# Optimization experiments

Measured on AMD Instinct MI355X. Metric: run time of the kernel, lower is better.

The kernel has to match this reference:

```python
import jax, jax.numpy as jnp
import numpy as np

N = 1536
NUM_SPECIES = 8
HIDDEN = 64
NUM_CENTERS = 32
CUTOFF = 5.0
RBF_GAMMA = 4.0  # 1 / width^2, width = 0.5
CENTERS = jnp.linspace(0.0, CUTOFF, NUM_CENTERS, dtype=jnp.float32)
PAIR_IN = NUM_CENTERS + HIDDEN                       # 96
LOCAL_IN = NUM_CENTERS * NUM_SPECIES + HIDDEN // 2 + 1  # 289


def cutoff_fn(d):
    x = jnp.clip(d / CUTOFF, 0.0, 1.0)
    return jnp.where(d < CUTOFF, 0.5 * (jnp.cos(jnp.pi * x) + 1.0), jnp.zeros_like(d))


def rbf_fn(d):
    return jnp.exp(-RBF_GAMMA * (d[..., None] - CENTERS) ** 2)


def mlp3(x, W1, b1, W2, b2, W3, b3):
    h = jax.nn.silu(x @ W1 + b1)
    h = jax.nn.silu(h @ W2 + b2)
    return h @ W3 + b3


def setup_inputs() -> dict:
    key = jax.random.key(0)
    ks = jax.random.split(key, 20)
    s = 0.1
    d = {
        "species": jax.random.randint(ks[0], (N,), 0, NUM_SPECIES, dtype=jnp.int32),
        "positions": jax.random.normal(ks[1], (N, 3), jnp.float32) * 4.0,
        "total_charge": jax.random.normal(ks[2], (1,), jnp.float32),
        "embed": jax.random.normal(ks[3], (NUM_SPECIES, HIDDEN // 2), jnp.float32) * s,
        "W1": jax.random.normal(ks[4], (PAIR_IN, HIDDEN), jnp.float32) * s,
        "b1": jnp.zeros((HIDDEN,), jnp.float32),
        "W2": jax.random.normal(ks[5], (HIDDEN, HIDDEN), jnp.float32) * s,
        "b2": jnp.zeros((HIDDEN,), jnp.float32),
        "W3": jax.random.normal(ks[6], (HIDDEN, 1), jnp.float32) * s,
        "b3": jnp.zeros((1,), jnp.float32),
        "atom_bias": jax.random.normal(ks[7], (NUM_SPECIES, 1), jnp.float32) * s,
        "cW1": jax.random.normal(ks[8], (LOCAL_IN, HIDDEN), jnp.float32) * s,
        "cb1": jnp.zeros((HIDDEN,), jnp.float32),
        "cW2": jax.random.normal(ks[9], (HIDDEN, HIDDEN), jnp.float32) * s,
        "cb2": jnp.zeros((HIDDEN,), jnp.float32),
        "cW3": jax.random.normal(ks[10], (HIDDEN, 1), jnp.float32) * s,
        "cb3": jnp.zeros((1,), jnp.float32),
        "charge_scale": jnp.float32(1.0),
        "coulomb_scale": jnp.float32(1.0),
        "softening_raw": jnp.float32(-3.0),
    }
    return d


def reference(species, positions, total_charge, embed, W1, b1, W2, b2, W3, b3,
              atom_bias, cW1, cb1, cW2, cb2, cW3, cb3,
              charge_scale, coulomb_scale, softening_raw):
    n = positions.shape[0]
    diff = positions[:, None, :] - positions[None, :, :]          # [n,n,3]
    dist = jnp.sqrt((diff ** 2).sum(-1) + 1e-12)                  # [n,n]
    iu0, iu1 = jnp.triu_indices(n, k=1)
    rij = dist[iu0, iu1]                                          # [P]
    cut = cutoff_fn(rij)
    ei = embed[species[iu0]]
    ej = embed[species[iu1]]
    pair_feat = jnp.concatenate([rbf_fn(rij), ei + ej, ei * ej], axis=-1)  # [P,96]
    pair_energy = mlp3(pair_feat, W1, b1, W2, b2, W3, b3)[:, 0]
    energy = jnp.sum(pair_energy * cut) + atom_bias[species].sum()

    # --- latent charges ---
    cut_mat = cutoff_fn(dist) * (1.0 - jnp.eye(n, dtype=dist.dtype))
    basis = rbf_fn(dist) * cut_mat[..., None]                     # [n,n,K]
    one_hot = jax.nn.one_hot(species, NUM_SPECIES, dtype=dist.dtype)
    local = jnp.einsum('ijk,jc->ick', basis, one_hot).reshape(n, -1)  # [n, S*K]
    x = jnp.concatenate([local, embed[species],
                         jnp.broadcast_to(total_charge, (n, 1))], axis=-1)
    raw = mlp3(x, cW1, cb1, cW2, cb2, cW3, cb3)[:, 0] * charge_scale
    charges = raw - raw.mean() + total_charge[0] / n
    soft = jax.nn.softplus(softening_raw) + 0.001
    energy_lr = coulomb_scale * jnp.sum(charges[iu0] * charges[iu1]
                                        / jnp.sqrt(rij ** 2 + soft ** 2))
    energy = energy + energy_lr
    return (energy, charges)
```

## Files before the change

### kernel.cpp

```cpp
#include <hip/hip_runtime.h>
#include <math.h>

#define NATOMS 1536
#define NSPEC 8
#define HID 64
#define NCEN 32
#define CUTOFF_R 5.0f
#define PI_F 3.14159265358979323846f
#define NBR_CAP 1024
#define MAXP 576
#define PREP_BLOCKS 65
#define PAIR_B NATOMS
#define TAIL_GRID (PAIR_B + 256)

typedef __attribute__((ext_vector_type(8))) short short8;
typedef __attribute__((ext_vector_type(4))) float float4v;

__device__ __forceinline__ float silu_f(float x) {
    return x / (1.f + __expf(-x));
}
__device__ __forceinline__ short f2bf(float x) {
    unsigned u = __float_as_uint(x);
    u += 0x7fffu + ((u >> 16) & 1u);
    return (short)(u >> 16);
}
__device__ __forceinline__ float cut_f(float d) {
    return 0.5f * (__cosf((PI_F / CUTOFF_R) * d) + 1.f);
}

__global__ __launch_bounds__(256) void k_one(
    const int* __restrict__ species, const float* __restrict__ pos,
    const float* __restrict__ tq, const float* __restrict__ embed,
    const float* __restrict__ cW1, const float* __restrict__ cb1,
    const float* __restrict__ cW2, const float* __restrict__ cb2,
    const float* __restrict__ cW3, const float* __restrict__ cb3,
    const float* __restrict__ charge_scale,
    const float* __restrict__ W1, const float* __restrict__ b1,
    const float* __restrict__ W2,
    float* __restrict__ ctab, short* __restrict__ bw1, short* __restrict__ bw2,
    float* __restrict__ raw,
    unsigned int* __restrict__ pnum, uint2* __restrict__ pdlist)
{
    __shared__ float2 dc_l[NBR_CAP];
    __shared__ unsigned short spj_l[NBR_CAP];
    __shared__ float s_part[8 * 256];
    __shared__ float s_x[292];
    __shared__ float s_h[64];
    __shared__ unsigned n_cnt, p_cnt;

    const int t = threadIdx.x;

    if (blockIdx.x >= NATOMS) {
        const int b = blockIdx.x - NATOMS;
        if (b < 64) {
            if (t < 64) {
                const int c = b;
                const int si2 = c >> 3, sj2 = c & 7;
                const int o = t;
                float acc = b1[o];
                #pragma unroll 4
                for (int k = 0; k < 32; k++) {
                    const float a = embed[si2 * 32 + k];
                    const float bb = embed[sj2 * 32 + k];
                    acc += (a + bb) * W1[(32 + k) * HID + o];
                    acc += (a * bb) * W1[(64 + k) * HID + o];
                }
                ctab[c * HID + o] = acc;
            }
        } else {
            for (int e = t; e < 2048; e += 256) {
                const int tile = e >> 9, L = (e >> 3) & 63, j = e & 7;
                const int k = (L >> 4) * 8 + j;
                const int n = tile * 16 + (L & 15);
                bw1[e] = f2bf(W1[k * HID + n]);
            }
            for (int e = t; e < 4096; e += 256) {
                const int ct = e >> 9, L = (e >> 3) & 63, j = e & 7;
                const int c = ct >> 2, tile = ct & 3;
                const int k = c * 32 + (L >> 4) * 8 + j;
                const int n = tile * 16 + (L & 15);
                bw2[e] = f2bf(W2[k * HID + n]);
            }
        }
        return;
    }

    const int i = blockIdx.x;
    const int lane = t & 63;
    if (t == 0) { n_cnt = 0u; p_cnt = 0u; }
    __syncthreads();

    const float xi = pos[3*i+0], yi = pos[3*i+1], zi = pos[3*i+2];
    const int si = species[i];

    #pragma unroll
    for (int j0 = 0; j0 < NATOMS; j0 += 256) {
        const int j = j0 + t;
        const float dx = xi - pos[3*j+0];
        const float dy = yi - pos[3*j+1];
        const float dz = zi - pos[3*j+2];
        const float d = sqrtf(dx*dx + dy*dy + dz*dz + 1e-12f);
        const bool within = (d < CUTOFF_R) && (j != i);
        const bool pair   = within && (j > i);
        const unsigned long long m  = __ballot((int)within);
        const unsigned long long mp = __ballot((int)pair);
        int spj = 0;
        if (within) {
            spj = species[j];
            const unsigned prefix = (unsigned)__popcll(m & ((1ull << lane) - 1ull));
            unsigned base = 0;
            if (prefix == 0) base = atomicAdd(&n_cnt, (unsigned)__popcll(m));
            base = (unsigned)__builtin_amdgcn_readfirstlane((int)base);
            const unsigned ofs = base + prefix;
            if (ofs < NBR_CAP) {
                dc_l[ofs] = make_float2(d, cut_f(d));
                spj_l[ofs] = (unsigned short)((spj << 11) | j);
            }
        }
        if (pair) {
            const unsigned pprefix = (unsigned)__popcll(mp & ((1ull << lane) - 1ull));
            unsigned pbase = 0;
            if (pprefix == 0) pbase = atomicAdd(&p_cnt, (unsigned)__popcll(mp));
            pbase = (unsigned)__builtin_amdgcn_readfirstlane((int)pbase);
            const unsigned ofs = pbase + pprefix;
            if (ofs < MAXP) {
                uint2 pd;
                pd.x = (((unsigned)si * 8u + (unsigned)spj) << 22)
                     | ((unsigned)i << 11) | (unsigned)j;
                pd.y = __float_as_uint(d);
                pdlist[i * MAXP + ofs] = pd;
            }
        }
    }
    __syncthreads();
    const unsigned cnt = (n_cnt < NBR_CAP) ? n_cnt : NBR_CAP;
    if (t == 0) pnum[i] = (p_cnt < MAXP) ? p_cnt : MAXP;

    {
        const int k = t & 31, gg = t >> 5;
        const float ck = (float)k * (CUTOFF_R / 31.f);
        float f0=0.f,f1=0.f,f2=0.f,f3=0.f,f4=0.f,f5=0.f,f6=0.f,f7=0.f;
        #pragma unroll 2
        for (unsigned n = (unsigned)gg; n < cnt; n += 8) {
            const float2 dc = dc_l[n];
            const float diff = dc.x - ck;
            const float v = __expf(-4.f * diff * diff) * dc.y;
            const int sp = (int)(spj_l[n] >> 11);
            f0 += (sp == 0) ? v : 0.f;
            f1 += (sp == 1) ? v : 0.f;
            f2 += (sp == 2) ? v : 0.f;
            f3 += (sp == 3) ? v : 0.f;
            f4 += (sp == 4) ? v : 0.f;
            f5 += (sp == 5) ? v : 0.f;
            f6 += (sp == 6) ? v : 0.f;
            f7 += (sp == 7) ? v : 0.f;
        }
        float* sp_g = &s_part[gg * 256 + k];
        sp_g[0*32] = f0; sp_g[1*32] = f1; sp_g[2*32] = f2; sp_g[3*32] = f3;
        sp_g[4*32] = f4; sp_g[5*32] = f5; sp_g[6*32] = f6; sp_g[7*32] = f7;
    }
    __syncthreads();
    {
        float acc = 0.f;
        #pragma unroll
        for (int g2 = 0; g2 < 8; g2++) acc += s_part[g2 * 256 + t];
        s_x[t] = acc;
        if (t < 32) s_x[256 + t] = embed[si * 32 + t];
        if (t == 0) s_x[288] = tq[0];
    }
    __syncthreads();

    {
        const int g3 = t >> 6, o = t & 63;
        const int k0 = g3 * 72;
        const int k1 = (g3 == 3) ? 289 : (k0 + 72);
        float acc = 0.f;
        #pragma unroll 8
        for (int k = k0; k < k1; k++) acc += s_x[k] * cW1[k * 64 + o];
        s_part[g3 * 64 + o] = acc;
    }
    __syncthreads();
    if (t < 64) {
        const float a = cb1[t] + s_part[t] + s_part[64 + t]
                      + s_part[128 + t] + s_part[192 + t];
        s_h[t] = silu_f(a);
    }
    __syncthreads();
    {
        const int g3 = t >> 6, o = t & 63;
        float acc = 0.f;
        #pragma unroll
        for (int kk = 0; kk < 16; kk++) {
            const int k = g3 * 16 + kk;
            acc += s_h[k] * cW2[k * 64 + o];
        }
        s_part[g3 * 64 + o] = acc;
    }
    __syncthreads();
    if (t < 64) {
        const float a = cb2[t] + s_part[t] + s_part[64 + t]
                      + s_part[128 + t] + s_part[192 + t];
        float v = silu_f(a) * cW3[t];
        #pragma unroll
        for (int off = 32; off > 0; off >>= 1) v += __shfl_down(v, off);
        if (t == 0)
            raw[i] = (v + cb3[0]) * charge_scale[0];
    }
}

__global__ __launch_bounds__(256, 4) void k_pairlr(
    const float* __restrict__ pos,
    const float* __restrict__ raw, const float* __restrict__ tq,
    const float* __restrict__ softening,
    const float* __restrict__ b2, const float* __restrict__ W3,
    const float* __restrict__ b3, const float* __restrict__ ctab,
    const short* __restrict__ bw1, const short* __restrict__ bw2,
    const unsigned int* __restrict__ pnum, const uint2* __restrict__ pdlist,
    double* __restrict__ epp, double* __restrict__ elp,
    float* __restrict__ charges)
{
    __shared__ float s_tp[4][16 * 66];
    __shared__ float s_red[256];
    const int t = threadIdx.x;
    const int lane = t & 63;

    if (blockIdx.x < PAIR_B) {
        const int a = blockIdx.x;
        const int wid = t >> 6;
        const int col = lane & 15;
        const int quad = lane >> 4;
        const unsigned pn = pnum[a];
        float esum = 0.f;

        if (pn > 0) {
            const short8* __restrict__ bw1v = (const short8*)bw1;
            const short8* __restrict__ bw2v = (const short8*)bw2;
            short8 w1f[4], w2f[8];
            #pragma unroll
            for (int t4 = 0; t4 < 4; t4++) w1f[t4] = bw1v[t4 * 64 + lane];
            #pragma unroll
            for (int q8 = 0; q8 < 8; q8++) w2f[q8] = bw2v[q8 * 64 + lane];
            float b2l[4], w3l[4];
            #pragma unroll
            for (int t4 = 0; t4 < 4; t4++) { b2l[t4] = b2[t4*16+col]; w3l[t4] = W3[t4*16+col]; }
            const float b3v = b3[0];
            const uint2* __restrict__ seg = pdlist + (size_t)a * MAXP;
            float* tb = &s_tp[wid][0];

            for (unsigned w = (unsigned)wid; w * 16u < pn; w += 4u) {
                unsigned p_idx = w * 16u + (unsigned)col;
                const bool valid = p_idx < pn;
                if (!valid) p_idx = pn - 1;
                const uint2 pd = seg[p_idx];
                const int combo = (int)(pd.x >> 22);
                const float d = __uint_as_float(pd.y);
                const float cut = valid ? cut_f(d) : 0.f;
                if (lane < 16) esum += b3v * cut;

                short8 a1f;
                #pragma unroll
                for (int jj = 0; jj < 8; jj++) {
                    const float ck = (float)(quad * 8 + jj) * (CUTOFF_R / 31.f);
                    const float diff = d - ck;
                    a1f[jj] = f2bf(__expf(-4.f * diff * diff));
                }

                int cmb[4]; float cutr[4];
                #pragma unroll
                for (int r = 0; r < 4; r++) {
                    const int p = quad * 4 + r;
                    cmb[r]  = __shfl(combo, p);
                    cutr[r] = __shfl(cut, p);
                }

                float4v acc[4];
                #pragma unroll
                for (int t4 = 0; t4 < 4; t4++) {
                    #pragma unroll
                    for (int r = 0; r < 4; r++)
                        acc[t4][r] = ctab[cmb[r] * HID + t4 * 16 + col];
                }
                #pragma unroll
                for (int t4 = 0; t4 < 4; t4++)
                    acc[t4] = __builtin_amdgcn_mfma_f32_16x16x32_bf16(a1f, w1f[t4], acc[t4], 0, 0, 0);

                #pragma unroll
                for (int t4 = 0; t4 < 4; t4++) {
                    #pragma unroll
                    for (int r = 0; r < 4; r++)
                        tb[(quad * 4 + r) * 66 + t4 * 16 + col] = silu_f(acc[t4][r]);
                }
                short8 a2f[2];
                #pragma unroll
                for (int c = 0; c < 2; c++) {
                    #pragma unroll
                    for (int jj = 0; jj < 8; jj++)
                        a2f[c][jj] = f2bf(tb[col * 66 + c * 32 + quad * 8 + jj]);
                }

                float4v acc2[4];
                #pragma unroll
                for (int t4 = 0; t4 < 4; t4++) {
                    acc2[t4][0] = b2l[t4]; acc2[t4][1] = b2l[t4];
                    acc2[t4][2] = b2l[t4]; acc2[t4][3] = b2l[t4];
                }
                #pragma unroll
                for (int c = 0; c < 2; c++) {
                    #pragma unroll
                    for (int t4 = 0; t4 < 4; t4++)
                        acc2[t4] = __builtin_amdgcn_mfma_f32_16x16x32_bf16(a2f[c], w2f[c*4+t4], acc2[t4], 0, 0, 0);
                }

                #pragma unroll
                for (int r = 0; r < 4; r++) {
                    float part = 0.f;
                    #pragma unroll
                    for (int t4 = 0; t4 < 4; t4++) part += silu_f(acc2[t4][r]) * w3l[t4];
                    esum += part * cutr[r];
                }
            }
        }

        s_red[t] = esum;
        __syncthreads();
        for (int s = 128; s > 0; s >>= 1) { if (t < s) s_red[t] += s_red[t + s]; __syncthreads(); }
        if (t == 0) epp[a] = (double)s_red[0];
    } else {
        const int b = blockIdx.x - PAIR_B;

        float macc = 0.f;
        for (int idx = t; idx < NATOMS; idx += 256) macc += raw[idx];
        s_red[t] = macc;
        __syncthreads();
        for (int s = 128; s > 0; s >>= 1) { if (t < s) s_red[t] += s_red[t + s]; __syncthreads(); }
        const float mean = s_red[0] / (float)NATOMS;
        const float add = tq[0] / (float)NATOMS;
        __syncthreads();

        const int gid = b * 256 + t;
        if (gid < NATOMS) charges[gid] = raw[gid] - mean + add;

        const float sr = softening[0];
        const float sp = ((sr > 20.f) ? sr : log1pf(__expf(sr))) + 0.001f;
        const float sp2 = sp * sp;
        float acc = 0.f;
        for (int i = b; i < NATOMS; i += 256) {
            const float xi = pos[3*i+0], yi = pos[3*i+1], zi = pos[3*i+2];
            const float qi = raw[i] - mean + add;
            for (int j = i + 1 + t; j < NATOMS; j += 256) {
                const float dx = xi - pos[3*j+0];
                const float dy = yi - pos[3*j+1];
                const float dz = zi - pos[3*j+2];
                const float d2 = dx*dx + dy*dy + dz*dz + 1e-12f;
                const float qj = raw[j] - mean + add;
                acc += qi * qj * rsqrtf(d2 + sp2);
            }
        }
        s_red[t] = acc;
        __syncthreads();
        for (int s = 128; s > 0; s >>= 1) { if (t < s) s_red[t] += s_red[t + s]; __syncthreads(); }
        if (t == 0) elp[b] = (double)s_red[0];
    }
}

__global__ __launch_bounds__(256) void k_final(
    const int* __restrict__ species, const float* __restrict__ atom_bias,
    const float* __restrict__ coulomb_scale,
    const double* __restrict__ epp, const double* __restrict__ elp,
    float* __restrict__ out_energy)
{
    __shared__ float s_red[256];
    __shared__ double s_redd[256];
    const int t = threadIdx.x;

    float bacc = 0.f;
    for (int idx = t; idx < NATOMS; idx += 256) bacc += atom_bias[species[idx]];
    s_red[t] = bacc;
    __syncthreads();
    for (int s = 128; s > 0; s >>= 1) { if (t < s) s_red[t] += s_red[t + s]; __syncthreads(); }

    const double cs = (double)coulomb_scale[0];
    double acc = 0.0;
    for (int idx = t; idx < PAIR_B; idx += 256) acc += epp[idx];
    acc += cs * elp[t];
    s_redd[t] = acc;
    __syncthreads();
    for (int s = 128; s > 0; s >>= 1) { if (t < s) s_redd[t] += s_redd[t + s]; __syncthreads(); }
    if (t == 0) out_energy[0] = (float)(s_redd[0] + (double)s_red[0]);
}

extern "C" void kernel_launch(void* const* d_in, const int* in_sizes, int n_in,
                              void* d_out, int out_size, void* d_ws, size_t ws_size,
                              hipStream_t stream) {
    const int*   species       = (const int*)d_in[0];
    const float* pos           = (const float*)d_in[1];
    const float* tq            = (const float*)d_in[2];
    const float* embed         = (const float*)d_in[3];
    const float* W1            = (const float*)d_in[4];
    const float* b1            = (const float*)d_in[5];
    const float* W2            = (const float*)d_in[6];
    const float* b2            = (const float*)d_in[7];
    const float* W3            = (const float*)d_in[8];
    const float* b3            = (const float*)d_in[9];
    const float* atom_bias     = (const float*)d_in[10];
    const float* cW1           = (const float*)d_in[11];
    const float* cb1           = (const float*)d_in[12];
    const float* cW2           = (const float*)d_in[13];
    const float* cb2           = (const float*)d_in[14];
    const float* cW3           = (const float*)d_in[15];
    const float* cb3           = (const float*)d_in[16];
    const float* charge_scale  = (const float*)d_in[17];
    const float* coulomb_scale = (const float*)d_in[18];
    const float* softening     = (const float*)d_in[19];

    char* ws = (char*)d_ws;
    float*    raw    = (float*)(ws + 64);
    float*    ctab   = (float*)(ws + 8192);
    short*    bw1    = (short*)(ws + 24576);
    short*    bw2    = (short*)(ws + 28672);
    double*   epp    = (double*)(ws + 36864);
    double*   elp    = (double*)(ws + 49152);
    unsigned* pnum   = (unsigned*)(ws + 51200);
    uint2*    pdlist = (uint2*)(ws + 57344);

    float* out     = (float*)d_out;
    float* charges = out + 1;

    k_one<<<NATOMS + PREP_BLOCKS, 256, 0, stream>>>(
        species, pos, tq, embed,
        cW1, cb1, cW2, cb2, cW3, cb3, charge_scale,
        W1, b1, W2, ctab, bw1, bw2,
        raw, pnum, pdlist);
    k_pairlr<<<TAIL_GRID, 256, 0, stream>>>(
        pos, raw, tq, softening,
        b2, W3, b3, ctab, bw1, bw2, pnum, pdlist,
        epp, elp, charges);
    k_final<<<1, 256, 0, stream>>>(
        species, atom_bias, coulomb_scale, epp, elp, out);
}
```

Before: 144.2 us.

## Fuse pair-energy MLP into per-atom neighbor kernel, keeping pair list in LDS

```diff
diff --git a/kernel.cpp b/kernel.cpp
--- a/kernel.cpp
+++ b/kernel.cpp
@@ -8,10 +8,6 @@
 #define CUTOFF_R 5.0f
 #define PI_F 3.14159265358979323846f
 #define NBR_CAP 1024
-#define MAXP 576
-#define PREP_BLOCKS 65
-#define PAIR_B NATOMS
-#define TAIL_GRID (PAIR_B + 256)
 
 typedef __attribute__((ext_vector_type(8))) short short8;
 typedef __attribute__((ext_vector_type(4))) float float4v;
@@ -28,7 +24,7 @@
     return 0.5f * (__cosf((PI_F / CUTOFF_R) * d) + 1.f);
 }
 
-__global__ __launch_bounds__(256) void k_one(
+__global__ __launch_bounds__(256) void k_all(
     const int* __restrict__ species, const float* __restrict__ pos,
     const float* __restrict__ tq, const float* __restrict__ embed,
     const float* __restrict__ cW1, const float* __restrict__ cb1,
@@ -36,57 +32,23 @@
     const float* __restrict__ cW3, const float* __restrict__ cb3,
     const float* __restrict__ charge_scale,
     const float* __restrict__ W1, const float* __restrict__ b1,
-    const float* __restrict__ W2,
-    float* __restrict__ ctab, short* __restrict__ bw1, short* __restrict__ bw2,
-    float* __restrict__ raw,
-    unsigned int* __restrict__ pnum, uint2* __restrict__ pdlist)
+    const float* __restrict__ W2, const float* __restrict__ b2,
+    const float* __restrict__ W3, const float* __restrict__ b3,
+    float* __restrict__ raw, double* __restrict__ epp)
 {
     __shared__ float2 dc_l[NBR_CAP];
     __shared__ unsigned short spj_l[NBR_CAP];
-    __shared__ float s_part[8 * 256];
+    __shared__ unsigned short pj_l[NBR_CAP];
+    __shared__ float s_big[4 * 16 * 66];
+    __shared__ float ctab_l[8 * 64];
     __shared__ float s_x[292];
     __shared__ float s_h[64];
+    __shared__ float s_red[256];
     __shared__ unsigned n_cnt, p_cnt;
 
     const int t = threadIdx.x;
-
-    if (blockIdx.x >= NATOMS) {
-        const int b = blockIdx.x - NATOMS;
-        if (b < 64) {
-            if (t < 64) {
-                const int c = b;
-                const int si2 = c >> 3, sj2 = c & 7;
-                const int o = t;
-                float acc = b1[o];
-                #pragma unroll 4
-                for (int k = 0; k < 32; k++) {
-                    const float a = embed[si2 * 32 + k];
-                    const float bb = embed[sj2 * 32 + k];
-                    acc += (a + bb) * W1[(32 + k) * HID + o];
-                    acc += (a * bb) * W1[(64 + k) * HID + o];
-                }
-                ctab[c * HID + o] = acc;
-            }
-        } else {
-            for (int e = t; e < 2048; e += 256) {
-                const int tile = e >> 9, L = (e >> 3) & 63, j = e & 7;
-                const int k = (L >> 4) * 8 + j;
-                const int n = tile * 16 + (L & 15);
-                bw1[e] = f2bf(W1[k * HID + n]);
-            }
-            for (int e = t; e < 4096; e += 256) {
-                const int ct = e >> 9, L = (e >> 3) & 63, j = e & 7;
-                const int c = ct >> 2, tile = ct & 3;
-                const int k = c * 32 + (L >> 4) * 8 + j;
-                const int n = tile * 16 + (L & 15);
-                bw2[e] = f2bf(W2[k * HID + n]);
-            }
-        }
-        return;
-    }
-
+    const int lane = t & 63;
     const int i = blockIdx.x;
-    const int lane = t & 63;
     if (t == 0) { n_cnt = 0u; p_cnt = 0u; }
     __syncthreads();
 
@@ -101,40 +63,33 @@
         const float dz = zi - pos[3*j+2];
         const float d = sqrtf(dx*dx + dy*dy + dz*dz + 1e-12f);
         const bool within = (d < CUTOFF_R) && (j != i);
-        const bool pair   = within && (j > i);
-        const unsigned long long m  = __ballot((int)within);
-        const unsigned long long mp = __ballot((int)pair);
-        int spj = 0;
+        const unsigned long long m = __ballot((int)within);
+        unsigned ofs = 0xffffffffu;
         if (within) {
-            spj = species[j];
+            const int spj = species[j];
             const unsigned prefix = (unsigned)__popcll(m & ((1ull << lane) - 1ull));
             unsigned base = 0;
             if (prefix == 0) base = atomicAdd(&n_cnt, (unsigned)__popcll(m));
             base = (unsigned)__builtin_amdgcn_readfirstlane((int)base);
-            const unsigned ofs = base + prefix;
+            ofs = base + prefix;
             if (ofs < NBR_CAP) {
                 dc_l[ofs] = make_float2(d, cut_f(d));
                 spj_l[ofs] = (unsigned short)((spj << 11) | j);
             }
         }
+        const bool pair = within && (j > i) && (ofs < NBR_CAP);
+        const unsigned long long mp = __ballot((int)pair);
         if (pair) {
             const unsigned pprefix = (unsigned)__popcll(mp & ((1ull << lane) - 1ull));
             unsigned pbase = 0;
             if (pprefix == 0) pbase = atomicAdd(&p_cnt, (unsigned)__popcll(mp));
             pbase = (unsigned)__builtin_amdgcn_readfirstlane((int)pbase);
-            const unsigned ofs = pbase + pprefix;
-            if (ofs < MAXP) {
-                uint2 pd;
-                pd.x = (((unsigned)si * 8u + (unsigned)spj) << 22)
-                     | ((unsigned)i << 11) | (unsigned)j;
-                pd.y = __float_as_uint(d);
-                pdlist[i * MAXP + ofs] = pd;
-            }
+            pj_l[pbase + pprefix] = (unsigned short)ofs;
         }
     }
     __syncthreads();
     const unsigned cnt = (n_cnt < NBR_CAP) ? n_cnt : NBR_CAP;
-    if (t == 0) pnum[i] = (p_cnt < MAXP) ? p_cnt : MAXP;
+    const unsigned pn  = p_cnt;
 
     {
         const int k = t & 31, gg = t >> 5;
@@ -155,15 +110,29 @@
             f6 += (sp == 6) ? v : 0.f;
             f7 += (sp == 7) ? v : 0.f;
         }
-        float* sp_g = &s_part[gg * 256 + k];
+        float* sp_g = &s_big[gg * 256 + k];
         sp_g[0*32] = f0; sp_g[1*32] = f1; sp_g[2*32] = f2; sp_g[3*32] = f3;
         sp_g[4*32] = f4; sp_g[5*32] = f5; sp_g[6*32] = f6; sp_g[7*32] = f7;
     }
+    {
+        const int o = t & 63;
+        for (int sj2 = (t >> 6); sj2 < 8; sj2 += 4) {
+            float acc = b1[o];
+            #pragma unroll 4
+            for (int k = 0; k < 32; k++) {
+                const float a = embed[si * 32 + k];
+                const float bb = embed[sj2 * 32 + k];
+                acc += (a + bb) * W1[(32 + k) * HID + o];
+                acc += (a * bb) * W1[(64 + k) * HID + o];
+            }
+            ctab_l[sj2 * 64 + o] = acc;
+        }
+    }
     __syncthreads();
     {
         float acc = 0.f;
         #pragma unroll
-        for (int g2 = 0; g2 < 8; g2++) acc += s_part[g2 * 256 + t];
+        for (int g2 = 0; g2 < 8; g2++) acc += s_big[g2 * 256 + t];
         s_x[t] = acc;
         if (t < 32) s_x[256 + t] = embed[si * 32 + t];
         if (t == 0) s_x[288] = tq[0];
@@ -177,12 +146,12 @@
         float acc = 0.f;
         #pragma unroll 8
         for (int k = k0; k < k1; k++) acc += s_x[k] * cW1[k * 64 + o];
-        s_part[g3 * 64 + o] = acc;
+        s_big[g3 * 64 + o] = acc;
     }
     __syncthreads();
     if (t < 64) {
-        const float a = cb1[t] + s_part[t] + s_part[64 + t]
-                      + s_part[128 + t] + s_part[192 + t];
+        const float a = cb1[t] + s_big[t] + s_big[64 + t]
+                      + s_big[128 + t] + s_big[192 + t];
         s_h[t] = silu_f(a);
     }
     __syncthreads();
@@ -194,173 +163,167 @@
             const int k = g3 * 16 + kk;
             acc += s_h[k] * cW2[k * 64 + o];
         }
-        s_part[g3 * 64 + o] = acc;
+        s_big[g3 * 64 + o] = acc;
     }
     __syncthreads();
     if (t < 64) {
-        const float a = cb2[t] + s_part[t] + s_part[64 + t]
-                      + s_part[128 + t] + s_part[192 + t];
+        const float a = cb2[t] + s_big[t] + s_big[64 + t]
+                      + s_big[128 + t] + s_big[192 + t];
         float v = silu_f(a) * cW3[t];
         #pragma unroll
         for (int off = 32; off > 0; off >>= 1) v += __shfl_down(v, off);
         if (t == 0)
             raw[i] = (v + cb3[0]) * charge_scale[0];
     }
-}
-
-__global__ __launch_bounds__(256, 4) void k_pairlr(
+    __syncthreads();
+
+    const int wid = t >> 6;
+    const int col = lane & 15;
+    const int quad = lane >> 4;
+    float esum = 0.f;
+
+    if (pn > 0) {
+        short8 w1f[4], w2f[8];
+        #pragma unroll
+        for (int t4 = 0; t4 < 4; t4++)
+            #pragma unroll
+            for (int jj = 0; jj < 8; jj++)
+                w1f[t4][jj] = f2bf(W1[((lane >> 4) * 8 + jj) * HID + t4 * 16 + (lane & 15)]);
+        #pragma unroll
+        for (int q8 = 0; q8 < 8; q8++)
+            #pragma unroll
+            for (int jj = 0; jj < 8; jj++)
+                w2f[q8][jj] = f2bf(W2[((q8 >> 2) * 32 + (lane >> 4) * 8 + jj) * HID
+                                      + (q8 & 3) * 16 + (lane & 15)]);
+        float b2l[4], w3l[4];
+        #pragma unroll
+        for (int t4 = 0; t4 < 4; t4++) { b2l[t4] = b2[t4*16+col]; w3l[t4] = W3[t4*16+col]; }
+        const float b3v = b3[0];
+        float* tb = &s_big[wid * 1056];
+
+        for (unsigned w = (unsigned)wid; w * 16u < pn; w += 4u) {
+            unsigned p_idx = w * 16u + (unsigned)col;
+            const bool valid = p_idx < pn;
+            if (!valid) p_idx = pn - 1;
+            const unsigned n = pj_l[p_idx];
+            const float2 dc = dc_l[n];
+            const float d = dc.x;
+            const int spj = (int)(spj_l[n] >> 11);
+            const float cut = valid ? dc.y : 0.f;
+            if (lane < 16) esum += b3v * cut;
+
+            short8 a1f;
+            #pragma unroll
+            for (int jj = 0; jj < 8; jj++) {
+                const float ck = (float)(quad * 8 + jj) * (CUTOFF_R / 31.f);
+                const float diff = d - ck;
+                a1f[jj] = f2bf(__expf(-4.f * diff * diff));
+            }
+
+            int cmb[4]; float cutr[4];
+            #pragma unroll
+            for (int r = 0; r < 4; r++) {
+                const int p = quad * 4 + r;
+                cmb[r]  = __shfl(spj, p);
+                cutr[r] = __shfl(cut, p);
+            }
+
+            float4v acc[4];
+            #pragma unroll
+            for (int t4 = 0; t4 < 4; t4++) {
+                #pragma unroll
+                for (int r = 0; r < 4; r++)
+                    acc[t4][r] = ctab_l[cmb[r] * HID + t4 * 16 + col];
+            }
+            #pragma unroll
+            for (int t4 = 0; t4 < 4; t4++)
+                acc[t4] = __builtin_amdgcn_mfma_f32_16x16x32_bf16(a1f, w1f[t4], acc[t4], 0, 0, 0);
+
+            #pragma unroll
+            for (int t4 = 0; t4 < 4; t4++) {
+                #pragma unroll
+                for (int r = 0; r < 4; r++)
+                    tb[(quad * 4 + r) * 66 + t4 * 16 + col] = silu_f(acc[t4][r]);
+            }
+            short8 a2f[2];
+            #pragma unroll
+            for (int c = 0; c < 2; c++) {
+                #pragma unroll
+                for (int jj = 0; jj < 8; jj++)
+                    a2f[c][jj] = f2bf(tb[col * 66 + c * 32 + quad * 8 + jj]);
+            }
+
+            float4v acc2[4];
+            #pragma unroll
+            for (int t4 = 0; t4 < 4; t4++) {
+                acc2[t4][0] = b2l[t4]; acc2[t4][1] = b2l[t4];
+                acc2[t4][2] = b2l[t4]; acc2[t4][3] = b2l[t4];
+            }
+            #pragma unroll
+            for (int c = 0; c < 2; c++) {
+                #pragma unroll
+                for (int t4 = 0; t4 < 4; t4++)
+                    acc2[t4] = __builtin_amdgcn_mfma_f32_16x16x32_bf16(a2f[c], w2f[c*4+t4], acc2[t4], 0, 0, 0);
+            }
+
+            #pragma unroll
+            for (int r = 0; r < 4; r++) {
+                float part = 0.f;
+                #pragma unroll
+                for (int t4 = 0; t4 < 4; t4++) part += silu_f(acc2[t4][r]) * w3l[t4];
+                esum += part * cutr[r];
+            }
+        }
+    }
+
+    s_red[t] = esum;
+    __syncthreads();
+    for (int s = 128; s > 0; s >>= 1) { if (t < s) s_red[t] += s_red[t + s]; __syncthreads(); }
+    if (t == 0) epp[i] = (double)s_red[0];
+}
+
+__global__ __launch_bounds__(256) void k_lr(
     const float* __restrict__ pos,
     const float* __restrict__ raw, const float* __restrict__ tq,
     const float* __restrict__ softening,
-    const float* __restrict__ b2, const float* __restrict__ W3,
-    const float* __restrict__ b3, const float* __restrict__ ctab,
-    const short* __restrict__ bw1, const short* __restrict__ bw2,
-    const unsigned int* __restrict__ pnum, const uint2* __restrict__ pdlist,
-    double* __restrict__ epp, double* __restrict__ elp,
-    float* __restrict__ charges)
+    double* __restrict__ elp, float* __restrict__ charges)
 {
-    __shared__ float s_tp[4][16 * 66];
     __shared__ float s_red[256];
     const int t = threadIdx.x;
-    const int lane = t & 63;
-
-    if (blockIdx.x < PAIR_B) {
-        const int a = blockIdx.x;
-        const int wid = t >> 6;
-        const int col = lane & 15;
-        const int quad = lane >> 4;
-        const unsigned pn = pnum[a];
-        float esum = 0.f;
-
-        if (pn > 0) {
-            const short8* __restrict__ bw1v = (const short8*)bw1;
-            const short8* __restrict__ bw2v = (const short8*)bw2;
-            short8 w1f[4], w2f[8];
-            #pragma unroll
-            for (int t4 = 0; t4 < 4; t4++) w1f[t4] = bw1v[t4 * 64 + lane];
-            #pragma unroll
-            for (int q8 = 0; q8 < 8; q8++) w2f[q8] = bw2v[q8 * 64 + lane];
-            float b2l[4], w3l[4];
-            #pragma unroll
-            for (int t4 = 0; t4 < 4; t4++) { b2l[t4] = b2[t4*16+col]; w3l[t4] = W3[t4*16+col]; }
-            const float b3v = b3[0];
-            const uint2* __restrict__ seg = pdlist + (size_t)a * MAXP;
-            float* tb = &s_tp[wid][0];
-
-            for (unsigned w = (unsigned)wid; w * 16u < pn; w += 4u) {
-                unsigned p_idx = w * 16u + (unsigned)col;
-                const bool valid = p_idx < pn;
-                if (!valid) p_idx = pn - 1;
-                const uint2 pd = seg[p_idx];
-                const int combo = (int)(pd.x >> 22);
-                const float d = __uint_as_float(pd.y);
-                const float cut = valid ? cut_f(d) : 0.f;
-                if (lane < 16) esum += b3v * cut;
-
-                short8 a1f;
-                #pragma unroll
-                for (int jj = 0; jj < 8; jj++) {
-                    const float ck = (float)(quad * 8 + jj) * (CUTOFF_R / 31.f);
-                    const float diff = d - ck;
-                    a1f[jj] = f2bf(__expf(-4.f * diff * diff));
-                }
-
-                int cmb[4]; float cutr[4];
-                #pragma unroll
-                for (int r = 0; r < 4; r++) {
-                    const int p = quad * 4 + r;
-                    cmb[r]  = __shfl(combo, p);
-                    cutr[r] = __shfl(cut, p);
-                }
-
-                float4v acc[4];
-                #pragma unroll
-                for (int t4 = 0; t4 < 4; t4++) {
-                    #pragma unroll
-                    for (int r = 0; r < 4; r++)
-                        acc[t4][r] = ctab[cmb[r] * HID + t4 * 16 + col];
-                }
-                #pragma unroll
-                for (int t4 = 0; t4 < 4; t4++)
-                    acc[t4] = __builtin_amdgcn_mfma_f32_16x16x32_bf16(a1f, w1f[t4], acc[t4], 0, 0, 0);
-
-                #pragma unroll
-                for (int t4 = 0; t4 < 4; t4++) {
-                    #pragma unroll
-                    for (int r = 0; r < 4; r++)
-                        tb[(quad * 4 + r) * 66 + t4 * 16 + col] = silu_f(acc[t4][r]);
-                }
-                short8 a2f[2];
-                #pragma unroll
-                for (int c = 0; c < 2; c++) {
-                    #pragma unroll
-                    for (int jj = 0; jj < 8; jj++)
-                        a2f[c][jj] = f2bf(tb[col * 66 + c * 32 + quad * 8 + jj]);
-                }
-
-                float4v acc2[4];
-                #pragma unroll
-                for (int t4 = 0; t4 < 4; t4++) {
-                    acc2[t4][0] = b2l[t4]; acc2[t4][1] = b2l[t4];
-                    acc2[t4][2] = b2l[t4]; acc2[t4][3] = b2l[t4];
-                }
-                #pragma unroll
-                for (int c = 0; c < 2; c++) {
-                    #pragma unroll
-                    for (int t4 = 0; t4 < 4; t4++)
-                        acc2[t4] = __builtin_amdgcn_mfma_f32_16x16x32_bf16(a2f[c], w2f[c*4+t4], acc2[t4], 0, 0, 0);
-                }
-
-                #pragma unroll
-                for (int r = 0; r < 4; r++) {
-                    float part = 0.f;
-                    #pragma unroll
-                    for (int t4 = 0; t4 < 4; t4++) part += silu_f(acc2[t4][r]) * w3l[t4];
-                    esum += part * cutr[r];
-                }
-            }
-        }
-
-        s_red[t] = esum;
-        __syncthreads();
-        for (int s = 128; s > 0; s >>= 1) { if (t < s) s_red[t] += s_red[t + s]; __syncthreads(); }
-        if (t == 0) epp[a] = (double)s_red[0];
-    } else {
-        const int b = blockIdx.x - PAIR_B;
-
-        float macc = 0.f;
-        for (int idx = t; idx < NATOMS; idx += 256) macc += raw[idx];
-        s_red[t] = macc;
-        __syncthreads();
-        for (int s = 128; s > 0; s >>= 1) { if (t < s) s_red[t] += s_red[t + s]; __syncthreads(); }
-        const float mean = s_red[0] / (float)NATOMS;
-        const float add = tq[0] / (float)NATOMS;
-        __syncthreads();
-
-        const int gid = b * 256 + t;
-        if (gid < NATOMS) charges[gid] = raw[gid] - mean + add;
-
-        const float sr = softening[0];
-        const float sp = ((sr > 20.f) ? sr : log1pf(__expf(sr))) + 0.001f;
-        const float sp2 = sp * sp;
-        float acc = 0.f;
-        for (int i = b; i < NATOMS; i += 256) {
-            const float xi = pos[3*i+0], yi = pos[3*i+1], zi = pos[3*i+2];
-            const float qi = raw[i] - mean + add;
-            for (int j = i + 1 + t; j < NATOMS; j += 256) {
-                const float dx = xi - pos[3*j+0];
-                const float dy = yi - pos[3*j+1];
-                const float dz = zi - pos[3*j+2];
-                const float d2 = dx*dx + dy*dy + dz*dz + 1e-12f;
-                const float qj = raw[j] - mean + add;
-                acc += qi * qj * rsqrtf(d2 + sp2);
-            }
-        }
-        s_red[t] = acc;
-        __syncthreads();
-        for (int s = 128; s > 0; s >>= 1) { if (t < s) s_red[t] += s_red[t + s]; __syncthreads(); }
-        if (t == 0) elp[b] = (double)s_red[0];
-    }
+    const int b = blockIdx.x;
+
+    float macc = 0.f;
+    for (int idx = t; idx < NATOMS; idx += 256) macc += raw[idx];
+    s_red[t] = macc;
+    __syncthreads();
+    for (int s = 128; s > 0; s >>= 1) { if (t < s) s_red[t] += s_red[t + s]; __syncthreads(); }
+    const float mean = s_red[0] / (float)NATOMS;
+    const float add = tq[0] / (float)NATOMS;
+    __syncthreads();
+
+    const int gid = b * 256 + t;
+    if (gid < NATOMS) charges[gid] = raw[gid] - mean + add;
+
+    const float sr = softening[0];
+    const float sp = ((sr > 20.f) ? sr : log1pf(__expf(sr))) + 0.001f;
+    const float sp2 = sp * sp;
+    float acc = 0.f;
+    for (int i = b; i < NATOMS; i += 256) {
+        const float xi = pos[3*i+0], yi = pos[3*i+1], zi = pos[3*i+2];
+        const float qi = raw[i] - mean + add;
+        for (int j = i + 1 + t; j < NATOMS; j += 256) {
+            const float dx = xi - pos[3*j+0];
+            const float dy = yi - pos[3*j+1];
+            const float dz = zi - pos[3*j+2];
+            const float d2 = dx*dx + dy*dy + dz*dz + 1e-12f;
+            const float qj = raw[j] - mean + add;
+            acc += qi * qj * rsqrtf(d2 + sp2);
+        }
+    }
+    s_red[t] = acc;
+    __syncthreads();
+    for (int s = 128; s > 0; s >>= 1) { if (t < s) s_red[t] += s_red[t + s]; __syncthreads(); }
+    if (t == 0) elp[b] = (double)s_red[0];
 }
 
 __global__ __launch_bounds__(256) void k_final(
@@ -381,7 +344,7 @@
 
     const double cs = (double)coulomb_scale[0];
     double acc = 0.0;
-    for (int idx = t; idx < PAIR_B; idx += 256) acc += epp[idx];
+    for (int idx = t; idx < NATOMS; idx += 256) acc += epp[idx];
     acc += cs * elp[t];
     s_redd[t] = acc;
     __syncthreads();
@@ -414,27 +377,20 @@
     const float* softening     = (const float*)d_in[19];
 
     char* ws = (char*)d_ws;
-    float*    raw    = (float*)(ws + 64);
-    float*    ctab   = (float*)(ws + 8192);
-    short*    bw1    = (short*)(ws + 24576);
-    short*    bw2    = (short*)(ws + 28672);
-    double*   epp    = (double*)(ws + 36864);
-    double*   elp    = (double*)(ws + 49152);
-    unsigned* pnum   = (unsigned*)(ws + 51200);
-    uint2*    pdlist = (uint2*)(ws + 57344);
+    float*  raw = (float*)(ws + 64);
+    double* epp = (double*)(ws + 8192);
+    double* elp = (double*)(ws + 20480);
 
     float* out     = (float*)d_out;
     float* charges = out + 1;
 
-    k_one<<<NATOMS + PREP_BLOCKS, 256, 0, stream>>>(
+    k_all<<<NATOMS, 256, 0, stream>>>(
         species, pos, tq, embed,
         cW1, cb1, cW2, cb2, cW3, cb3, charge_scale,
-        W1, b1, W2, ctab, bw1, bw2,
-        raw, pnum, pdlist);
-    k_pairlr<<<TAIL_GRID, 256, 0, stream>>>(
-        pos, raw, tq, softening,
-        b2, W3, b3, ctab, bw1, bw2, pnum, pdlist,
-        epp, elp, charges);
+        W1, b1, W2, b2, W3, b3,
+        raw, epp);
+    k_lr<<<256, 256, 0, stream>>>(
+        pos, raw, tq, softening, elp, charges);
     k_final<<<1, 256, 0, stream>>>(
         species, atom_bias, coulomb_scale, epp, elp, out);
 }
```

Measured after the change: 160.5 us. 1.11x slower.

## Replace per-pair MLP evaluation with tabulated distance lookup per species combo

Applied to the files above, without the earlier changes.

```diff
diff --git a/kernel.cpp b/kernel.cpp
--- a/kernel.cpp
+++ b/kernel.cpp
@@ -9,9 +9,9 @@
 #define PI_F 3.14159265358979323846f
 #define NBR_CAP 1024
 #define MAXP 576
-#define PREP_BLOCKS 65
-#define PAIR_B NATOMS
-#define TAIL_GRID (PAIR_B + 256)
+#define NPTS 2048
+#define PREP_BLOCKS 64
+#define TAIL_GRID 256
 
 typedef __attribute__((ext_vector_type(8))) short short8;
 typedef __attribute__((ext_vector_type(4))) float float4v;
@@ -36,57 +36,135 @@
     const float* __restrict__ cW3, const float* __restrict__ cb3,
     const float* __restrict__ charge_scale,
     const float* __restrict__ W1, const float* __restrict__ b1,
-    const float* __restrict__ W2,
-    float* __restrict__ ctab, short* __restrict__ bw1, short* __restrict__ bw2,
-    float* __restrict__ raw,
+    const float* __restrict__ W2, const float* __restrict__ b2,
+    const float* __restrict__ W3, const float* __restrict__ b3,
+    float* __restrict__ etab, float* __restrict__ raw,
     unsigned int* __restrict__ pnum, uint2* __restrict__ pdlist)
 {
-    __shared__ float2 dc_l[NBR_CAP];
-    __shared__ unsigned short spj_l[NBR_CAP];
-    __shared__ float s_part[8 * 256];
+    __shared__ __align__(16) unsigned char smem[18432];
     __shared__ float s_x[292];
     __shared__ float s_h[64];
     __shared__ unsigned n_cnt, p_cnt;
 
     const int t = threadIdx.x;
+    const int lane = t & 63;
 
     if (blockIdx.x >= NATOMS) {
-        const int b = blockIdx.x - NATOMS;
-        if (b < 64) {
-            if (t < 64) {
-                const int c = b;
-                const int si2 = c >> 3, sj2 = c & 7;
-                const int o = t;
-                float acc = b1[o];
-                #pragma unroll 4
-                for (int k = 0; k < 32; k++) {
-                    const float a = embed[si2 * 32 + k];
-                    const float bb = embed[sj2 * 32 + k];
-                    acc += (a + bb) * W1[(32 + k) * HID + o];
-                    acc += (a * bb) * W1[(64 + k) * HID + o];
-                }
-                ctab[c * HID + o] = acc;
-            }
-        } else {
-            for (int e = t; e < 2048; e += 256) {
-                const int tile = e >> 9, L = (e >> 3) & 63, j = e & 7;
-                const int k = (L >> 4) * 8 + j;
-                const int n = tile * 16 + (L & 15);
-                bw1[e] = f2bf(W1[k * HID + n]);
-            }
-            for (int e = t; e < 4096; e += 256) {
-                const int ct = e >> 9, L = (e >> 3) & 63, j = e & 7;
-                const int c = ct >> 2, tile = ct & 3;
-                const int k = c * 32 + (L >> 4) * 8 + j;
-                const int n = tile * 16 + (L & 15);
-                bw2[e] = f2bf(W2[k * HID + n]);
+        const int c = blockIdx.x - NATOMS;
+        float* sm_f = (float*)smem;
+        float* ctab_l = sm_f + 4 * 1056;
+
+        if (t < 64) {
+            const int si2 = c >> 3, sj2 = c & 7;
+            const int o = t;
+            float acc = b1[o];
+            #pragma unroll 4
+            for (int k = 0; k < 32; k++) {
+                const float a = embed[si2 * 32 + k];
+                const float bb = embed[sj2 * 32 + k];
+                acc += (a + bb) * W1[(32 + k) * HID + o];
+                acc += (a * bb) * W1[(64 + k) * HID + o];
+            }
+            ctab_l[o] = acc;
+        }
+        __syncthreads();
+
+        const int wid = t >> 6;
+        const int col = lane & 15;
+        const int quad = lane >> 4;
+
+        short8 w1f[4], w2f[8];
+        #pragma unroll
+        for (int t4 = 0; t4 < 4; t4++)
+            #pragma unroll
+            for (int jj = 0; jj < 8; jj++)
+                w1f[t4][jj] = f2bf(W1[((lane >> 4) * 8 + jj) * HID + t4 * 16 + col]);
+        #pragma unroll
+        for (int q8 = 0; q8 < 8; q8++)
+            #pragma unroll
+            for (int jj = 0; jj < 8; jj++)
+                w2f[q8][jj] = f2bf(W2[((q8 >> 2) * 32 + (lane >> 4) * 8 + jj) * HID
+                                      + (q8 & 3) * 16 + col]);
+        float b2l[4], w3l[4];
+        #pragma unroll
+        for (int t4 = 0; t4 < 4; t4++) { b2l[t4] = b2[t4*16+col]; w3l[t4] = W3[t4*16+col]; }
+        const float b3v = b3[0];
+        float* tb = sm_f + wid * 1056;
+        const float dstep = CUTOFF_R / (float)(NPTS - 1);
+
+        for (int tp = 0; tp < 32; tp++) {
+            const int p0 = wid * 512 + tp * 16;
+            const float d = (float)(p0 + col) * dstep;
+            const float cut = cut_f(d);
+
+            short8 a1f;
+            #pragma unroll
+            for (int jj = 0; jj < 8; jj++) {
+                const float ck = (float)(quad * 8 + jj) * (CUTOFF_R / 31.f);
+                const float diff = d - ck;
+                a1f[jj] = f2bf(__expf(-4.f * diff * diff));
+            }
+            float cutr[4];
+            #pragma unroll
+            for (int r = 0; r < 4; r++) cutr[r] = __shfl(cut, quad * 4 + r);
+
+            float4v acc[4];
+            #pragma unroll
+            for (int t4 = 0; t4 < 4; t4++) {
+                #pragma unroll
+                for (int r = 0; r < 4; r++) acc[t4][r] = ctab_l[t4 * 16 + col];
+            }
+            #pragma unroll
+            for (int t4 = 0; t4 < 4; t4++)
+                acc[t4] = __builtin_amdgcn_mfma_f32_16x16x32_bf16(a1f, w1f[t4], acc[t4], 0, 0, 0);
+
+            #pragma unroll
+            for (int t4 = 0; t4 < 4; t4++) {
+                #pragma unroll
+                for (int r = 0; r < 4; r++)
+                    tb[(quad * 4 + r) * 66 + t4 * 16 + col] = silu_f(acc[t4][r]);
+            }
+            short8 a2f[2];
+            #pragma unroll
+            for (int cc = 0; cc < 2; cc++) {
+                #pragma unroll
+                for (int jj = 0; jj < 8; jj++)
+                    a2f[cc][jj] = f2bf(tb[col * 66 + cc * 32 + quad * 8 + jj]);
+            }
+            float4v acc2[4];
+            #pragma unroll
+            for (int t4 = 0; t4 < 4; t4++) {
+                acc2[t4][0] = b2l[t4]; acc2[t4][1] = b2l[t4];
+                acc2[t4][2] = b2l[t4]; acc2[t4][3] = b2l[t4];
+            }
+            #pragma unroll
+            for (int cc = 0; cc < 2; cc++) {
+                #pragma unroll
+                for (int t4 = 0; t4 < 4; t4++)
+                    acc2[t4] = __builtin_amdgcn_mfma_f32_16x16x32_bf16(a2f[cc], w2f[cc*4+t4], acc2[t4], 0, 0, 0);
+            }
+
+            #pragma unroll
+            for (int r = 0; r < 4; r++) {
+                float part = 0.f;
+                #pragma unroll
+                for (int t4 = 0; t4 < 4; t4++) part += silu_f(acc2[t4][r]) * w3l[t4];
+                part += __shfl_xor(part, 1);
+                part += __shfl_xor(part, 2);
+                part += __shfl_xor(part, 4);
+                part += __shfl_xor(part, 8);
+                if (col == 0)
+                    etab[c * NPTS + p0 + quad * 4 + r] = (part + b3v) * cutr[r];
             }
         }
         return;
     }
 
+    float2* dc_l = (float2*)smem;
+    unsigned short* spj_l = (unsigned short*)(smem + 8192);
+    float* s_part = (float*)(smem + 10240);
+
     const int i = blockIdx.x;
-    const int lane = t & 63;
     if (t == 0) { n_cnt = 0u; p_cnt = 0u; }
     __syncthreads();
 
@@ -208,165 +286,82 @@
     }
 }
 
-__global__ __launch_bounds__(256, 4) void k_pairlr(
+__global__ __launch_bounds__(256) void k_tail(
     const float* __restrict__ pos,
     const float* __restrict__ raw, const float* __restrict__ tq,
     const float* __restrict__ softening,
-    const float* __restrict__ b2, const float* __restrict__ W3,
-    const float* __restrict__ b3, const float* __restrict__ ctab,
-    const short* __restrict__ bw1, const short* __restrict__ bw2,
+    const float* __restrict__ etab,
     const unsigned int* __restrict__ pnum, const uint2* __restrict__ pdlist,
-    double* __restrict__ epp, double* __restrict__ elp,
+    double* __restrict__ epsum, double* __restrict__ elp,
     float* __restrict__ charges)
 {
-    __shared__ float s_tp[4][16 * 66];
     __shared__ float s_red[256];
     const int t = threadIdx.x;
-    const int lane = t & 63;
-
-    if (blockIdx.x < PAIR_B) {
-        const int a = blockIdx.x;
-        const int wid = t >> 6;
-        const int col = lane & 15;
-        const int quad = lane >> 4;
-        const unsigned pn = pnum[a];
-        float esum = 0.f;
-
-        if (pn > 0) {
-            const short8* __restrict__ bw1v = (const short8*)bw1;
-            const short8* __restrict__ bw2v = (const short8*)bw2;
-            short8 w1f[4], w2f[8];
-            #pragma unroll
-            for (int t4 = 0; t4 < 4; t4++) w1f[t4] = bw1v[t4 * 64 + lane];
-            #pragma unroll
-            for (int q8 = 0; q8 < 8; q8++) w2f[q8] = bw2v[q8 * 64 + lane];
-            float b2l[4], w3l[4];
-            #pragma unroll
-            for (int t4 = 0; t4 < 4; t4++) { b2l[t4] = b2[t4*16+col]; w3l[t4] = W3[t4*16+col]; }
-            const float b3v = b3[0];
+    const int b = blockIdx.x;
+
+    {
+        const float iscale = (float)(NPTS - 1) / CUTOFF_R;
+        float acc = 0.f;
+        for (int a = b; a < NATOMS; a += 256) {
+            const unsigned pn = pnum[a];
             const uint2* __restrict__ seg = pdlist + (size_t)a * MAXP;
-            float* tb = &s_tp[wid][0];
-
-            for (unsigned w = (unsigned)wid; w * 16u < pn; w += 4u) {
-                unsigned p_idx = w * 16u + (unsigned)col;
-                const bool valid = p_idx < pn;
-                if (!valid) p_idx = pn - 1;
-                const uint2 pd = seg[p_idx];
+            for (unsigned p = (unsigned)t; p < pn; p += 256) {
+                const uint2 pd = seg[p];
                 const int combo = (int)(pd.x >> 22);
                 const float d = __uint_as_float(pd.y);
-                const float cut = valid ? cut_f(d) : 0.f;
-                if (lane < 16) esum += b3v * cut;
-
-                short8 a1f;
-                #pragma unroll
-                for (int jj = 0; jj < 8; jj++) {
-                    const float ck = (float)(quad * 8 + jj) * (CUTOFF_R / 31.f);
-                    const float diff = d - ck;
-                    a1f[jj] = f2bf(__expf(-4.f * diff * diff));
-                }
-
-                int cmb[4]; float cutr[4];
-                #pragma unroll
-                for (int r = 0; r < 4; r++) {
-                    const int p = quad * 4 + r;
-                    cmb[r]  = __shfl(combo, p);
-                    cutr[r] = __shfl(cut, p);
-                }
-
-                float4v acc[4];
-                #pragma unroll
-                for (int t4 = 0; t4 < 4; t4++) {
-                    #pragma unroll
-                    for (int r = 0; r < 4; r++)
-                        acc[t4][r] = ctab[cmb[r] * HID + t4 * 16 + col];
-                }
-                #pragma unroll
-                for (int t4 = 0; t4 < 4; t4++)
-                    acc[t4] = __builtin_amdgcn_mfma_f32_16x16x32_bf16(a1f, w1f[t4], acc[t4], 0, 0, 0);
-
-                #pragma unroll
-                for (int t4 = 0; t4 < 4; t4++) {
-                    #pragma unroll
-                    for (int r = 0; r < 4; r++)
-                        tb[(quad * 4 + r) * 66 + t4 * 16 + col] = silu_f(acc[t4][r]);
-                }
-                short8 a2f[2];
-                #pragma unroll
-                for (int c = 0; c < 2; c++) {
-                    #pragma unroll
-                    for (int jj = 0; jj < 8; jj++)
-                        a2f[c][jj] = f2bf(tb[col * 66 + c * 32 + quad * 8 + jj]);
-                }
-
-                float4v acc2[4];
-                #pragma unroll
-                for (int t4 = 0; t4 < 4; t4++) {
-                    acc2[t4][0] = b2l[t4]; acc2[t4][1] = b2l[t4];
-                    acc2[t4][2] = b2l[t4]; acc2[t4][3] = b2l[t4];
-                }
-                #pragma unroll
-                for (int c = 0; c < 2; c++) {
-                    #pragma unroll
-                    for (int t4 = 0; t4 < 4; t4++)
-                        acc2[t4] = __builtin_amdgcn_mfma_f32_16x16x32_bf16(a2f[c], w2f[c*4+t4], acc2[t4], 0, 0, 0);
-                }
-
-                #pragma unroll
-                for (int r = 0; r < 4; r++) {
-                    float part = 0.f;
-                    #pragma unroll
-                    for (int t4 = 0; t4 < 4; t4++) part += silu_f(acc2[t4][r]) * w3l[t4];
-                    esum += part * cutr[r];
-                }
-            }
-        }
-
-        s_red[t] = esum;
-        __syncthreads();
-        for (int s = 128; s > 0; s >>= 1) { if (t < s) s_red[t] += s_red[t + s]; __syncthreads(); }
-        if (t == 0) epp[a] = (double)s_red[0];
-    } else {
-        const int b = blockIdx.x - PAIR_B;
-
-        float macc = 0.f;
-        for (int idx = t; idx < NATOMS; idx += 256) macc += raw[idx];
-        s_red[t] = macc;
-        __syncthreads();
-        for (int s = 128; s > 0; s >>= 1) { if (t < s) s_red[t] += s_red[t + s]; __syncthreads(); }
-        const float mean = s_red[0] / (float)NATOMS;
-        const float add = tq[0] / (float)NATOMS;
-        __syncthreads();
-
-        const int gid = b * 256 + t;
-        if (gid < NATOMS) charges[gid] = raw[gid] - mean + add;
-
-        const float sr = softening[0];
-        const float sp = ((sr > 20.f) ? sr : log1pf(__expf(sr))) + 0.001f;
-        const float sp2 = sp * sp;
-        float acc = 0.f;
-        for (int i = b; i < NATOMS; i += 256) {
-            const float xi = pos[3*i+0], yi = pos[3*i+1], zi = pos[3*i+2];
-            const float qi = raw[i] - mean + add;
-            for (int j = i + 1 + t; j < NATOMS; j += 256) {
-                const float dx = xi - pos[3*j+0];
-                const float dy = yi - pos[3*j+1];
-                const float dz = zi - pos[3*j+2];
-                const float d2 = dx*dx + dy*dy + dz*dz + 1e-12f;
-                const float qj = raw[j] - mean + add;
-                acc += qi * qj * rsqrtf(d2 + sp2);
+                const float fidx = d * iscale;
+                const int k = (int)fidx;
+                const float frac = fidx - (float)k;
+                const float t0 = etab[combo * NPTS + k];
+                const float t1 = etab[combo * NPTS + k + 1];
+                acc += t0 + (t1 - t0) * frac;
             }
         }
         s_red[t] = acc;
         __syncthreads();
         for (int s = 128; s > 0; s >>= 1) { if (t < s) s_red[t] += s_red[t + s]; __syncthreads(); }
-        if (t == 0) elp[b] = (double)s_red[0];
-    }
+        if (t == 0) epsum[b] = (double)s_red[0];
+        __syncthreads();
+    }
+
+    float macc = 0.f;
+    for (int idx = t; idx < NATOMS; idx += 256) macc += raw[idx];
+    s_red[t] = macc;
+    __syncthreads();
+    for (int s = 128; s > 0; s >>= 1) { if (t < s) s_red[t] += s_red[t + s]; __syncthreads(); }
+    const float mean = s_red[0] / (float)NATOMS;
+    const float add = tq[0] / (float)NATOMS;
+    __syncthreads();
+
+    const int gid = b * 256 + t;
+    if (gid < NATOMS) charges[gid] = raw[gid] - mean + add;
+
+    const float sr = softening[0];
+    const float sp = ((sr > 20.f) ? sr : log1pf(__expf(sr))) + 0.001f;
+    const float sp2 = sp * sp;
+    float acc = 0.f;
+    for (int i = b; i < NATOMS; i += 256) {
+        const float xi = pos[3*i+0], yi = pos[3*i+1], zi = pos[3*i+2];
+        const float qi = raw[i] - mean + add;
+        for (int j = i + 1 + t; j < NATOMS; j += 256) {
+            const float dx = xi - pos[3*j+0];
+            const float dy = yi - pos[3*j+1];
+            const float dz = zi - pos[3*j+2];
+            const float d2 = dx*dx + dy*dy + dz*dz + 1e-12f;
+            const float qj = raw[j] - mean + add;
+            acc += qi * qj * rsqrtf(d2 + sp2);
+        }
+    }
+    s_red[t] = acc;
+    __syncthreads();
+    for (int s = 128; s > 0; s >>= 1) { if (t < s) s_red[t] += s_red[t + s]; __syncthreads(); }
+    if (t == 0) elp[b] = (double)s_red[0];
 }
 
 __global__ __launch_bounds__(256) void k_final(
     const int* __restrict__ species, const float* __restrict__ atom_bias,
     const float* __restrict__ coulomb_scale,
-    const double* __restrict__ epp, const double* __restrict__ elp,
+    const double* __restrict__ epsum, const double* __restrict__ elp,
     float* __restrict__ out_energy)
 {
     __shared__ float s_red[256];
@@ -380,9 +375,7 @@
     for (int s = 128; s > 0; s >>= 1) { if (t < s) s_red[t] += s_red[t + s]; __syncthreads(); }
 
     const double cs = (double)coulomb_scale[0];
-    double acc = 0.0;
-    for (int idx = t; idx < PAIR_B; idx += 256) acc += epp[idx];
-    acc += cs * elp[t];
+    double acc = epsum[t] + cs * elp[t];
     s_redd[t] = acc;
     __syncthreads();
     for (int s = 128; s > 0; s >>= 1) { if (t < s) s_redd[t] += s_redd[t + s]; __syncthreads(); }
@@ -415,13 +408,11 @@
 
     char* ws = (char*)d_ws;
     float*    raw    = (float*)(ws + 64);
-    float*    ctab   = (float*)(ws + 8192);
-    short*    bw1    = (short*)(ws + 24576);
-    short*    bw2    = (short*)(ws + 28672);
-    double*   epp    = (double*)(ws + 36864);
-    double*   elp    = (double*)(ws + 49152);
-    unsigned* pnum   = (unsigned*)(ws + 51200);
-    uint2*    pdlist = (uint2*)(ws + 57344);
+    double*   epsum  = (double*)(ws + 8192);
+    double*   elp    = (double*)(ws + 10240);
+    unsigned* pnum   = (unsigned*)(ws + 12288);
+    float*    etab   = (float*)(ws + 20480);
+    uint2*    pdlist = (uint2*)(ws + 544768);
 
     float* out     = (float*)d_out;
     float* charges = out + 1;
@@ -429,12 +420,11 @@
     k_one<<<NATOMS + PREP_BLOCKS, 256, 0, stream>>>(
         species, pos, tq, embed,
         cW1, cb1, cW2, cb2, cW3, cb3, charge_scale,
-        W1, b1, W2, ctab, bw1, bw2,
-        raw, pnum, pdlist);
-    k_pairlr<<<TAIL_GRID, 256, 0, stream>>>(
-        pos, raw, tq, softening,
-        b2, W3, b3, ctab, bw1, bw2, pnum, pdlist,
-        epp, elp, charges);
+        W1, b1, W2, b2, W3, b3,
+        etab, raw, pnum, pdlist);
+    k_tail<<<TAIL_GRID, 256, 0, stream>>>(
+        pos, raw, tq, softening, etab, pnum, pdlist,
+        epsum, elp, charges);
     k_final<<<1, 256, 0, stream>>>(
-        species, atom_bias, coulomb_scale, epp, elp, out);
-}
+        species, atom_bias, coulomb_scale, epsum, elp, out);
+}
```

New measurement: 220.3 us. 1.53x slower.
